# Kernel optimization log

Hardware: AMD Instinct MI355X
Metric: run time of the kernel (lower is better)

Reference implementation:

```python
import jax, jax.numpy as jnp
import numpy as np

N_NODES = 50000
N_EDGES = 800000
IN_DIM = 64
HID = 64
OUT_DIM = 40
NEG_SLOPE = 0.2


def _gat_layer(x, src, dst, W, b, att, bias, n_nodes):
    # x: [N, Fin] -> lin -> [N, Fout]; heads = 1
    h = x @ W.T + b
    x_i = h[dst]                      # [E, F] target features
    x_j = h[src]                      # [E, F] source features
    # edge attention logits: cat([x_i, x_j]) @ att.T -> [E, 1]
    alpha = jnp.concatenate([x_i, x_j], axis=-1) @ att.T
    alpha = jax.nn.leaky_relu(alpha, NEG_SLOPE)
    # segment softmax over destination node (pyg_utils.softmax)
    amax = jax.ops.segment_max(alpha, dst, num_segments=n_nodes)
    e = jnp.exp(alpha - amax[dst])
    denom = jax.ops.segment_sum(e, dst, num_segments=n_nodes)
    alpha = e / (denom[dst] + 1e-16)
    # message = alpha * x_j, aggr='add' scatter to dst, then + bias
    out = jax.ops.segment_sum(x_j * alpha, dst, num_segments=n_nodes)
    return out + bias


def setup_inputs() -> dict:
    key = jax.random.key(0)
    ks = jax.random.split(key, 12)
    x = jax.random.normal(ks[0], (N_NODES, IN_DIM), dtype=jnp.float32)
    edge_index = jax.random.randint(ks[1], (2, N_EDGES), 0, N_NODES, dtype=jnp.int64)
    def glorot(k, shape):
        fan_in, fan_out = shape[1], shape[0]
        lim = float(np.sqrt(6.0 / (fan_in + fan_out)))
        return jax.random.uniform(k, shape, jnp.float32, -lim, lim)
    W1 = glorot(ks[2], (HID, IN_DIM))
    b1 = jnp.zeros((HID,), jnp.float32)
    att1 = glorot(ks[3], (1, 2 * HID))
    bias1 = jnp.zeros((HID,), jnp.float32)
    W2 = glorot(ks[4], (HID, HID))
    b2 = jnp.zeros((HID,), jnp.float32)
    att2 = glorot(ks[5], (1, 2 * HID))
    bias2 = jnp.zeros((HID,), jnp.float32)
    Wp1 = glorot(ks[6], (HID, HID))
    bp1 = jnp.zeros((HID,), jnp.float32)
    Wp2 = glorot(ks[7], (OUT_DIM, HID))
    bp2 = jnp.zeros((OUT_DIM,), jnp.float32)
    return {"x": x, "edge_index": edge_index,
            "W1": W1, "b1": b1, "att1": att1, "bias1": bias1,
            "W2": W2, "b2": b2, "att2": att2, "bias2": bias2,
            "Wp1": Wp1, "bp1": bp1, "Wp2": Wp2, "bp2": bp2}


def reference(x, edge_index, W1, b1, att1, bias1, W2, b2, att2, bias2,
              Wp1, bp1, Wp2, bp2):
    src, dst = edge_index[0], edge_index[1]
    n = x.shape[0]
    # layer 1 (GAT) + relu; dropout p=0 in eval -> identity
    h = jax.nn.relu(_gat_layer(x, src, dst, W1, b1, att1, bias1, n))
    # layer 2 (GAT) + relu
    h = jax.nn.relu(_gat_layer(h, src, dst, W2, b2, att2, bias2, n))
    # post-MP MLP + log_softmax over classes
    h = h @ Wp1.T + bp1
    logits = h @ Wp2.T + bp2
    return jax.nn.log_softmax(logits, axis=1)
```

## Files before the change

### kernel.cpp

```cpp
#include <hip/hip_runtime.h>
#include <hip/hip_fp16.h>
#include <math.h>

#define NN 50000
#define NE 800000
#define NEG 0.2f

#define NPB 128
#define CHK 6250
#define NBUK 98
#define LCAP 10240
#define GB 782

typedef __attribute__((ext_vector_type(8))) short short8v;
typedef __attribute__((ext_vector_type(4))) float f32x4;

__device__ __forceinline__ float lrelu(float x){ return x > 0.f ? x : NEG * x; }

__device__ __forceinline__ float bcastf(float v, int l){
    return __uint_as_float(__builtin_amdgcn_readlane(__float_as_uint(v), l));
}
__device__ __forceinline__ short bf16t(float x){ return (short)(__float_as_uint(x) >> 16); }
__device__ __forceinline__ float bf16tof(short s){
    return __uint_as_float(((unsigned)(unsigned short)s) << 16);
}

__device__ __forceinline__ void lin_body(int blk, int tid,
                                         const float* __restrict__ X,
                                         const float* __restrict__ W,
                                         const float* __restrict__ b,
                                         const float* __restrict__ att,
                                         __half* __restrict__ Hh,
                                         float* __restrict__ ad,
                                         float* __restrict__ as_, int n){
    int lane = tid & 63, wid = tid >> 6;
    int nb = blk * 64 + wid * 16;
    if (nb >= n) return;
    int r0 = lane & 15, rg = lane >> 4;

    short8v a_hi[2], a_lo[2];
    int arow = nb + r0; if (arow >= n) arow = n - 1;
    const float* xp = X + (size_t)arow * 64 + rg * 8;
    #pragma unroll
    for (int ks = 0; ks < 2; ++ks){
        #pragma unroll
        for (int j = 0; j < 8; ++j){
            float v = xp[ks * 32 + j];
            short h = bf16t(v);
            a_hi[ks][j] = h;
            a_lo[ks][j] = bf16t(v - bf16tof(h));
        }
    }

    f32x4 acc[4] = {{0,0,0,0},{0,0,0,0},{0,0,0,0},{0,0,0,0}};
    #pragma unroll
    for (int nt = 0; nt < 4; ++nt){
        const float* wp = W + (size_t)(nt * 16 + r0) * 64 + rg * 8;
        #pragma unroll
        for (int ks = 0; ks < 2; ++ks){
            short8v b_hi, b_lo;
            #pragma unroll
            for (int j = 0; j < 8; ++j){
                float v = wp[ks * 32 + j];
                short h = bf16t(v);
                b_hi[j] = h;
                b_lo[j] = bf16t(v - bf16tof(h));
            }
            acc[nt] = __builtin_amdgcn_mfma_f32_16x16x32_bf16(a_hi[ks], b_hi, acc[nt], 0, 0, 0);
            acc[nt] = __builtin_amdgcn_mfma_f32_16x16x32_bf16(a_hi[ks], b_lo, acc[nt], 0, 0, 0);
            acc[nt] = __builtin_amdgcn_mfma_f32_16x16x32_bf16(a_lo[ks], b_hi, acc[nt], 0, 0, 0);
        }
    }

    #pragma unroll
    for (int nt = 0; nt < 4; ++nt){
        float bb = b[nt * 16 + r0];
        #pragma unroll
        for (int q = 0; q < 4; ++q){
            int node = nb + rg * 4 + q;
            float v = acc[nt][q] + bb;
            acc[nt][q] = v;
            if (node < n) Hh[(size_t)node * 64 + nt * 16 + r0] = __float2half(v);
        }
    }

    float attd[4], atts[4];
    #pragma unroll
    for (int nt = 0; nt < 4; ++nt){
        attd[nt] = att[nt * 16 + r0];
        atts[nt] = att[64 + nt * 16 + r0];
    }
    #pragma unroll
    for (int q = 0; q < 4; ++q){
        float pd = 0.f, ps = 0.f;
        #pragma unroll
        for (int nt = 0; nt < 4; ++nt){
            pd = fmaf(attd[nt], acc[nt][q], pd);
            ps = fmaf(atts[nt], acc[nt][q], ps);
        }
        #pragma unroll
        for (int off = 8; off; off >>= 1){
            pd += __shfl_xor(pd, off);
            ps += __shfl_xor(ps, off);
        }
        int node = nb + rg * 4 + q;
        if (r0 == 0 && node < n){ ad[node] = pd; as_[node] = ps; }
    }
}

__global__ __launch_bounds__(256) void k_fuse0(const float* __restrict__ X,
                                               const float* __restrict__ W1,
                                               const float* __restrict__ b1,
                                               const float* __restrict__ att1,
                                               __half* __restrict__ Hh,
                                               float* __restrict__ ad,
                                               float* __restrict__ as_,
                                               const int* __restrict__ dst,
                                               int* __restrict__ counts,
                                               const float* __restrict__ Wp1,
                                               const float* __restrict__ bp1,
                                               const float* __restrict__ Wp2,
                                               const float* __restrict__ bp2,
                                               float* __restrict__ Wc,
                                               float* __restrict__ bc){
    __shared__ int c[NBUK];
    int tid = threadIdx.x, blk = blockIdx.x;
    if (blk < GB){
        lin_body(blk, tid, X, W1, b1, att1, Hh, ad, as_, NN);
    } else if (blk < GB + NPB){
        int cb = blk - GB;
        for (int i = tid; i < NBUK; i += 256) c[i] = 0;
        __syncthreads();
        int beg = cb * CHK, end = min(beg + CHK, NE);
        for (int i = beg + tid; i < end; i += 256) atomicAdd(&c[dst[i] >> 9], 1);
        __syncthreads();
        for (int i = tid; i < NBUK; i += 256) counts[i * NPB + cb] = c[i];
    } else {
        for (int idx = tid; idx < 2560; idx += 256){
            int cc = idx >> 6, k = idx & 63;
            float s = 0.f;
            #pragma unroll 8
            for (int j = 0; j < 64; ++j) s = fmaf(Wp2[cc * 64 + j], Wp1[j * 64 + k], s);
            Wc[idx] = s;
        }
        if (tid < 40){
            float s = bp2[tid];
            for (int j = 0; j < 64; ++j) s = fmaf(Wp2[tid * 64 + j], bp1[j], s);
            bc[tid] = s;
        }
    }
}

__global__ __launch_bounds__(NPB) void k_scan1(int* __restrict__ counts,
                                               int* __restrict__ tot){
    __shared__ int wsum[2];
    int b = blockIdx.x, tid = threadIdx.x, lane = tid & 63, wid = tid >> 6;
    int v = counts[b * NPB + tid];
    int incl = v;
    #pragma unroll
    for (int off = 1; off < 64; off <<= 1){
        int t = __shfl_up(incl, off);
        if (lane >= off) incl += t;
    }
    if (lane == 63) wsum[wid] = incl;
    __syncthreads();
    int excl = incl - v + (wid ? wsum[0] : 0);
    counts[b * NPB + tid] = excl;
    if (tid == NPB - 1) tot[b] = excl + v;
}

__global__ __launch_bounds__(128) void k_scan2(const int* __restrict__ tot,
                                               int* __restrict__ bbase){
    __shared__ int wsum[2];
    int tid = threadIdx.x, lane = tid & 63, wid = tid >> 6;
    int v = (tid < NBUK) ? tot[tid] : 0;
    int incl = v;
    #pragma unroll
    for (int off = 1; off < 64; off <<= 1){
        int t = __shfl_up(incl, off);
        if (lane >= off) incl += t;
    }
    if (lane == 63) wsum[wid] = incl;
    __syncthreads();
    int excl = incl - v + (wid ? wsum[0] : 0);
    if (tid < NBUK) bbase[tid] = excl;
    if (tid == NBUK - 1) bbase[NBUK] = excl + v;
}

__global__ __launch_bounds__(256) void k_partC(const int* __restrict__ src,
                                               const int* __restrict__ dst,
                                               const int* __restrict__ cofs,
                                               const int* __restrict__ bbase,
                                               unsigned* __restrict__ part){
    __shared__ int lcur[NBUK];
    int tid = threadIdx.x, blk = blockIdx.x;
    for (int i = tid; i < NBUK; i += 256) lcur[i] = bbase[i] + cofs[i * NPB + blk];
    __syncthreads();
    int beg = blk * CHK, end = min(beg + CHK, NE);
    for (int i = beg + tid; i < end; i += 256){
        int d = dst[i];
        int pos = atomicAdd(&lcur[d >> 9], 1);
        part[pos] = ((unsigned)(d & 511) << 16) | (unsigned)src[i];
    }
}

__global__ __launch_bounds__(256) void k_buildD(const unsigned* __restrict__ part,
                                                const int* __restrict__ bbase,
                                                int* __restrict__ rowstart,
                                                int* __restrict__ csr){
    __shared__ int hist[512], cur[512];
    __shared__ int csrbuf[LCAP];
    __shared__ int swave[4];
    int tid = threadIdx.x, lane = tid & 63, wid = tid >> 6;
    int b = blockIdx.x;
    int ebeg = bbase[b], eend = bbase[b + 1], cnt = eend - ebeg;

    for (int i = tid; i < 512; i += 256) hist[i] = 0;
    __syncthreads();
    for (int i = tid; i < cnt; i += 256) atomicAdd(&hist[part[ebeg + i] >> 16], 1);
    __syncthreads();

    int h0 = hist[2 * tid], h1 = hist[2 * tid + 1];
    int v = h0 + h1, incl = v;
    #pragma unroll
    for (int off = 1; off < 64; off <<= 1){
        int t = __shfl_up(incl, off);
        if (lane >= off) incl += t;
    }
    if (lane == 63) swave[wid] = incl;
    __syncthreads();
    int woff = 0;
    #pragma unroll
    for (int w = 0; w < 4; ++w) if (w < wid) woff += swave[w];
    int e0 = woff + incl - v;
    int e1 = e0 + h0;
    cur[2 * tid] = e0; cur[2 * tid + 1] = e1;
    int gi = b * 512 + 2 * tid;
    if (gi     <= NN) rowstart[gi]     = ebeg + e0;
    if (gi + 1 <= NN) rowstart[gi + 1] = ebeg + e1;
    __syncthreads();

    for (int i = tid; i < cnt; i += 256){
        unsigned u = part[ebeg + i];
        int lp = atomicAdd(&cur[u >> 16], 1);
        if (lp < LCAP) csrbuf[lp] = (int)(u & 0xFFFFu);
    }
    __syncthreads();
    int m = min(cnt, LCAP);
    for (int i = tid; i < m; i += 256) csr[ebeg + i] = csrbuf[i];
}

__global__ __launch_bounds__(256) void k_lin_mfma(const float* __restrict__ X,
                                                  const float* __restrict__ W,
                                                  const float* __restrict__ b,
                                                  const float* __restrict__ att,
                                                  __half* __restrict__ Hh,
                                                  float* __restrict__ ad,
                                                  float* __restrict__ as_, int n){
    lin_body(blockIdx.x, threadIdx.x, X, W, b, att, Hh, ad, as_, n);
}

__global__ __launch_bounds__(256) void k_agg(const __half2* __restrict__ H2,
                                             const float* __restrict__ ad,
                                             const float* __restrict__ as_,
                                             const int* __restrict__ rowstart,
                                             const int* __restrict__ csr,
                                             const float2* __restrict__ bias2,
                                             float2* __restrict__ OUT2, int n){
    int tid = threadIdx.x, lane = tid & 63, wid = tid >> 6;
    int node = blockIdx.x * 4 + wid;
    if (node >= n) return;
    int beg = rowstart[node], end = rowstart[node + 1];
    float adn = ad[node];
    int half = lane >> 5, hl = lane & 31;

    float accx = 0.f, accy = 0.f, denom = 0.f;
    for (int cbeg = beg; cbeg < end; cbeg += 64){
        int k = cbeg + lane;
        int s = (k < end) ? csr[k] : 0;
        float e = (k < end) ? __expf(lrelu(adn + as_[s])) : 0.f;
        float es = e;
        #pragma unroll
        for (int off = 32; off; off >>= 1) es += __shfl_xor(es, off);
        denom += es;
        int cnt = min(64, end - cbeg);
        int j = 0;
        for (; j + 8 <= cnt; j += 8){
            int i0 = j + half, i1 = j + 2 + half, i2 = j + 4 + half, i3 = j + 6 + half;
            int   s0 = __shfl(s, i0), s1 = __shfl(s, i1), s2 = __shfl(s, i2), s3 = __shfl(s, i3);
            float e0 = __shfl(e, i0), e1 = __shfl(e, i1), e2 = __shfl(e, i2), e3 = __shfl(e, i3);
            __half2 ha = H2[(size_t)s0 * 32 + hl];
            __half2 hb = H2[(size_t)s1 * 32 + hl];
            __half2 hc = H2[(size_t)s2 * 32 + hl];
            __half2 hd = H2[(size_t)s3 * 32 + hl];
            float2 fa = __half22float2(ha), fb = __half22float2(hb);
            float2 fc = __half22float2(hc), fd = __half22float2(hd);
            accx = fmaf(e0, fa.x, accx); accy = fmaf(e0, fa.y, accy);
            accx = fmaf(e1, fb.x, accx); accy = fmaf(e1, fb.y, accy);
            accx = fmaf(e2, fc.x, accx); accy = fmaf(e2, fc.y, accy);
            accx = fmaf(e3, fd.x, accx); accy = fmaf(e3, fd.y, accy);
        }
        for (; j + 4 <= cnt; j += 4){
            int i0 = j + half, i1 = j + 2 + half;
            int   s0 = __shfl(s, i0), s1 = __shfl(s, i1);
            float e0 = __shfl(e, i0), e1 = __shfl(e, i1);
            float2 fa = __half22float2(H2[(size_t)s0 * 32 + hl]);
            float2 fb = __half22float2(H2[(size_t)s1 * 32 + hl]);
            accx = fmaf(e0, fa.x, accx); accy = fmaf(e0, fa.y, accy);
            accx = fmaf(e1, fb.x, accx); accy = fmaf(e1, fb.y, accy);
        }
        for (; j < cnt; j += 2){
            int idx = j + half;
            int   se = __shfl(s, idx);
            float ee = __shfl(e, idx);
            float2 f = __half22float2(H2[(size_t)se * 32 + hl]);
            accx = fmaf(ee, f.x, accx); accy = fmaf(ee, f.y, accy);
        }
    }
    accx += __shfl_xor(accx, 32);
    accy += __shfl_xor(accy, 32);
    if (half == 0){
        float2 bb = bias2[hl];
        float inv = 1.f / (denom + 1e-16f);
        float2 o;
        o.x = fmaxf(fmaf(accx, inv, bb.x), 0.f);
        o.y = fmaxf(fmaf(accy, inv, bb.y), 0.f);
        OUT2[(size_t)node * 32 + hl] = o;
    }
}

__global__ __launch_bounds__(256) void k_mlp_mfma(const float* __restrict__ G,
                                                  const float* __restrict__ Wc,
                                                  const float* __restrict__ bc,
                                                  float* __restrict__ out, int n){
    int lane = threadIdx.x & 63, wid = threadIdx.x >> 6;
    int nb = blockIdx.x * 64 + wid * 16;
    if (nb >= n) return;
    int r0 = lane & 15, rg = lane >> 4;

    short8v a_hi[2], a_lo[2];
    int arow = nb + r0; if (arow >= n) arow = n - 1;
    const float* gp = G + (size_t)arow * 64 + rg * 8;
    #pragma unroll
    for (int ks = 0; ks < 2; ++ks){
        #pragma unroll
        for (int j = 0; j < 8; ++j){
            float v = gp[ks * 32 + j];
            short h = bf16t(v);
            a_hi[ks][j] = h;
            a_lo[ks][j] = bf16t(v - bf16tof(h));
        }
    }

    f32x4 acc[3] = {{0,0,0,0},{0,0,0,0},{0,0,0,0}};
    #pragma unroll
    for (int nt = 0; nt < 3; ++nt){
        int f = nt * 16 + r0;
        int fr = (f < 40) ? f : 39;
        const float* wp = Wc + (size_t)fr * 64 + rg * 8;
        #pragma unroll
        for (int ks = 0; ks < 2; ++ks){
            short8v b_hi, b_lo;
            #pragma unroll
            for (int j = 0; j < 8; ++j){
                float v = wp[ks * 32 + j];
                short h = bf16t(v);
                b_hi[j] = h;
                b_lo[j] = bf16t(v - bf16tof(h));
            }
            acc[nt] = __builtin_amdgcn_mfma_f32_16x16x32_bf16(a_hi[ks], b_hi, acc[nt], 0, 0, 0);
            acc[nt] = __builtin_amdgcn_mfma_f32_16x16x32_bf16(a_hi[ks], b_lo, acc[nt], 0, 0, 0);
            acc[nt] = __builtin_amdgcn_mfma_f32_16x16x32_bf16(a_lo[ks], b_hi, acc[nt], 0, 0, 0);
        }
    }

    float bcv[3];
    #pragma unroll
    for (int nt = 0; nt < 3; ++nt){
        int f = nt * 16 + r0;
        bcv[nt] = (f < 40) ? bc[f] : 0.f;
    }

    #pragma unroll
    for (int q = 0; q < 4; ++q){
        int node = nb + rg * 4 + q;
        float l0 = acc[0][q] + bcv[0];
        float l1 = acc[1][q] + bcv[1];
        float l2 = (32 + r0 < 40) ? acc[2][q] + bcv[2] : -INFINITY;
        float m = fmaxf(l0, fmaxf(l1, l2));
        #pragma unroll
        for (int off = 8; off; off >>= 1) m = fmaxf(m, __shfl_xor(m, off));
        float s = __expf(l0 - m) + __expf(l1 - m) + ((32 + r0 < 40) ? __expf(l2 - m) : 0.f);
        #pragma unroll
        for (int off = 8; off; off >>= 1) s += __shfl_xor(s, off);
        float lse = m + __logf(s);
        if (node < n){
            out[(size_t)node * 40 + r0]      = l0 - lse;
            out[(size_t)node * 40 + 16 + r0] = l1 - lse;
            if (32 + r0 < 40) out[(size_t)node * 40 + 32 + r0] = l2 - lse;
        }
    }
}

extern "C" void kernel_launch(void* const* d_in, const int* in_sizes, int n_in,
                              void* d_out, int out_size, void* d_ws, size_t ws_size,
                              hipStream_t stream){
    const float* x     = (const float*)d_in[0];
    const int*   ei    = (const int*)  d_in[1];
    const float* W1    = (const float*)d_in[2];
    const float* b1    = (const float*)d_in[3];
    const float* att1  = (const float*)d_in[4];
    const float* bias1 = (const float*)d_in[5];
    const float* W2    = (const float*)d_in[6];
    const float* b2    = (const float*)d_in[7];
    const float* att2  = (const float*)d_in[8];
    const float* bias2 = (const float*)d_in[9];
    const float* Wp1   = (const float*)d_in[10];
    const float* bp1   = (const float*)d_in[11];
    const float* Wp2   = (const float*)d_in[12];
    const float* bp2   = (const float*)d_in[13];
    float* out = (float*)d_out;

    float*    base     = (float*)d_ws;
    float*    g        = base;
    __half*   hh       = (__half*)(base + 3200000);
    unsigned* part     = (unsigned*)(base + 4800000);
    int*      csr      = (int*)(base + 5600000);
    int*      counts   = (int*)(base + 6400000);
    int*      tot      = (int*)(base + 6412944);
    int*      bbase    = (int*)(base + 6413072);
    int*      rowstart = (int*)(base + 6413200);
    float*    ad       = base + 6463208;
    float*    as_      = base + 6513208;
    float*    Wc       = base + 6563208;
    float*    bc       = base + 6565768;

    const int* srcv = ei;
    const int* dstv = ei + NE;

    k_fuse0 <<<GB + NPB + 1, 256, 0, stream>>>(x, W1, b1, att1, hh, ad, as_,
                                               dstv, counts,
                                               Wp1, bp1, Wp2, bp2, Wc, bc);
    k_scan1 <<<NBUK, NPB, 0, stream>>>(counts, tot);
    k_scan2 <<<1, 128, 0, stream>>>(tot, bbase);
    k_partC <<<NPB, 256, 0, stream>>>(srcv, dstv, counts, bbase, part);
    k_buildD<<<NBUK, 256, 0, stream>>>(part, bbase, rowstart, csr);

    int nb = (NN + 3) / 4;
    k_agg     <<<nb, 256, 0, stream>>>((const __half2*)hh, ad, as_, rowstart, csr,
                                       (const float2*)bias1, (float2*)g, NN);
    k_lin_mfma<<<GB, 256, 0, stream>>>(g, W2, b2, att2, hh, ad, as_, NN);
    k_agg     <<<nb, 256, 0, stream>>>((const __half2*)hh, ad, as_, rowstart, csr,
                                       (const float2*)bias2, (float2*)g, NN);
    k_mlp_mfma<<<GB, 256, 0, stream>>>(g, Wc, bc, out, NN);
}
```

Before: 146.7 us.

## Fold bucket-base scan into partition kernels and stage edge data in LDS

Removes the single-block k_scan2 launch by having k_partC and k_buildD each recompute the 98-entry bucket base prefix sum redundantly in shared memory. In the aggregation kernel, per-edge source indices and attention weights are written to LDS and read back instead of broadcast with shuffles. The inner tail loops are collapsed into one 8-step loop that relies on zero-padded entries. This saves a kernel launch and some shuffle instructions, at the cost of redundant scan work per block and extra LDS traffic. Padded slots gather row 0 with weight zero, adding some wasted loads.

New measurement: 142.1 us. 3.1% less time.

```diff
diff --git a/kernel.cpp b/kernel.cpp
--- a/kernel.cpp
+++ b/kernel.cpp
@@ -17,9 +17,6 @@
 
 __device__ __forceinline__ float lrelu(float x){ return x > 0.f ? x : NEG * x; }
 
-__device__ __forceinline__ float bcastf(float v, int l){
-    return __uint_as_float(__builtin_amdgcn_readlane(__float_as_uint(v), l));
-}
 __device__ __forceinline__ short bf16t(float x){ return (short)(__float_as_uint(x) >> 16); }
 __device__ __forceinline__ float bf16tof(short s){
     return __uint_as_float(((unsigned)(unsigned short)s) << 16);
@@ -169,32 +166,36 @@
     if (tid == NPB - 1) tot[b] = excl + v;
 }
 
-__global__ __launch_bounds__(128) void k_scan2(const int* __restrict__ tot,
-                                               int* __restrict__ bbase){
-    __shared__ int wsum[2];
-    int tid = threadIdx.x, lane = tid & 63, wid = tid >> 6;
-    int v = (tid < NBUK) ? tot[tid] : 0;
-    int incl = v;
-    #pragma unroll
-    for (int off = 1; off < 64; off <<= 1){
-        int t = __shfl_up(incl, off);
-        if (lane >= off) incl += t;
-    }
-    if (lane == 63) wsum[wid] = incl;
-    __syncthreads();
-    int excl = incl - v + (wid ? wsum[0] : 0);
-    if (tid < NBUK) bbase[tid] = excl;
-    if (tid == NBUK - 1) bbase[NBUK] = excl + v;
+__device__ __forceinline__ void bbase_scan(const int* __restrict__ tot,
+                                           int* bb, int* wsum, int tid){
+    int lane = tid & 63, w2 = tid >> 6;
+    int vv = 0, incl = 0;
+    if (tid < 128){
+        vv = (tid < NBUK) ? tot[tid] : 0;
+        incl = vv;
+        #pragma unroll
+        for (int off = 1; off < 64; off <<= 1){
+            int t = __shfl_up(incl, off);
+            if (lane >= off) incl += t;
+        }
+        if (lane == 63) wsum[w2] = incl;
+    }
+    __syncthreads();
+    if (tid < NBUK) bb[tid] = incl - vv + (w2 ? wsum[0] : 0);
+    __syncthreads();
 }
 
 __global__ __launch_bounds__(256) void k_partC(const int* __restrict__ src,
                                                const int* __restrict__ dst,
                                                const int* __restrict__ cofs,
-                                               const int* __restrict__ bbase,
+                                               const int* __restrict__ tot,
                                                unsigned* __restrict__ part){
     __shared__ int lcur[NBUK];
+    __shared__ int bb[NBUK];
+    __shared__ int wsum[2];
     int tid = threadIdx.x, blk = blockIdx.x;
-    for (int i = tid; i < NBUK; i += 256) lcur[i] = bbase[i] + cofs[i * NPB + blk];
+    bbase_scan(tot, bb, wsum, tid);
+    for (int i = tid; i < NBUK; i += 256) lcur[i] = bb[i] + cofs[i * NPB + blk];
     __syncthreads();
     int beg = blk * CHK, end = min(beg + CHK, NE);
     for (int i = beg + tid; i < end; i += 256){
@@ -205,15 +206,18 @@
 }
 
 __global__ __launch_bounds__(256) void k_buildD(const unsigned* __restrict__ part,
-                                                const int* __restrict__ bbase,
+                                                const int* __restrict__ tot,
                                                 int* __restrict__ rowstart,
                                                 int* __restrict__ csr){
     __shared__ int hist[512], cur[512];
     __shared__ int csrbuf[LCAP];
     __shared__ int swave[4];
+    __shared__ int bb[NBUK];
+    __shared__ int wsum2[2];
     int tid = threadIdx.x, lane = tid & 63, wid = tid >> 6;
     int b = blockIdx.x;
-    int ebeg = bbase[b], eend = bbase[b + 1], cnt = eend - ebeg;
+    bbase_scan(tot, bb, wsum2, tid);
+    int ebeg = bb[b], cnt = tot[b];
 
     for (int i = tid; i < 512; i += 256) hist[i] = 0;
     __syncthreads();
@@ -267,6 +271,8 @@
                                              const int* __restrict__ csr,
                                              const float2* __restrict__ bias2,
                                              float2* __restrict__ OUT2, int n){
+    __shared__ float e_sh[4][64];
+    __shared__ int   s_sh[4][64];
     int tid = threadIdx.x, lane = tid & 63, wid = tid >> 6;
     int node = blockIdx.x * 4 + wid;
     if (node >= n) return;
@@ -277,44 +283,30 @@
     float accx = 0.f, accy = 0.f, denom = 0.f;
     for (int cbeg = beg; cbeg < end; cbeg += 64){
         int k = cbeg + lane;
-        int s = (k < end) ? csr[k] : 0;
-        float e = (k < end) ? __expf(lrelu(adn + as_[s])) : 0.f;
+        bool valid = (k < end);
+        int s = valid ? csr[k] : 0;
+        float e = valid ? __expf(lrelu(adn + as_[s])) : 0.f;
+        e_sh[wid][lane] = e;
+        s_sh[wid][lane] = valid ? s : 0;
         float es = e;
         #pragma unroll
         for (int off = 32; off; off >>= 1) es += __shfl_xor(es, off);
         denom += es;
         int cnt = min(64, end - cbeg);
-        int j = 0;
-        for (; j + 8 <= cnt; j += 8){
+        for (int j = 0; j < cnt; j += 8){
             int i0 = j + half, i1 = j + 2 + half, i2 = j + 4 + half, i3 = j + 6 + half;
-            int   s0 = __shfl(s, i0), s1 = __shfl(s, i1), s2 = __shfl(s, i2), s3 = __shfl(s, i3);
-            float e0 = __shfl(e, i0), e1 = __shfl(e, i1), e2 = __shfl(e, i2), e3 = __shfl(e, i3);
-            __half2 ha = H2[(size_t)s0 * 32 + hl];
-            __half2 hb = H2[(size_t)s1 * 32 + hl];
-            __half2 hc = H2[(size_t)s2 * 32 + hl];
-            __half2 hd = H2[(size_t)s3 * 32 + hl];
-            float2 fa = __half22float2(ha), fb = __half22float2(hb);
-            float2 fc = __half22float2(hc), fd = __half22float2(hd);
+            int   s0 = s_sh[wid][i0], s1 = s_sh[wid][i1];
+            int   s2 = s_sh[wid][i2], s3 = s_sh[wid][i3];
+            float e0 = e_sh[wid][i0], e1 = e_sh[wid][i1];
+            float e2 = e_sh[wid][i2], e3 = e_sh[wid][i3];
+            float2 fa = __half22float2(H2[(size_t)s0 * 32 + hl]);
+            float2 fb = __half22float2(H2[(size_t)s1 * 32 + hl]);
+            float2 fc = __half22float2(H2[(size_t)s2 * 32 + hl]);
+            float2 fd = __half22float2(H2[(size_t)s3 * 32 + hl]);
             accx = fmaf(e0, fa.x, accx); accy = fmaf(e0, fa.y, accy);
             accx = fmaf(e1, fb.x, accx); accy = fmaf(e1, fb.y, accy);
             accx = fmaf(e2, fc.x, accx); accy = fmaf(e2, fc.y, accy);
             accx = fmaf(e3, fd.x, accx); accy = fmaf(e3, fd.y, accy);
-        }
-        for (; j + 4 <= cnt; j += 4){
-            int i0 = j + half, i1 = j + 2 + half;
-            int   s0 = __shfl(s, i0), s1 = __shfl(s, i1);
-            float e0 = __shfl(e, i0), e1 = __shfl(e, i1);
-            float2 fa = __half22float2(H2[(size_t)s0 * 32 + hl]);
-            float2 fb = __half22float2(H2[(size_t)s1 * 32 + hl]);
-            accx = fmaf(e0, fa.x, accx); accy = fmaf(e0, fa.y, accy);
-            accx = fmaf(e1, fb.x, accx); accy = fmaf(e1, fb.y, accy);
-        }
-        for (; j < cnt; j += 2){
-            int idx = j + half;
-            int   se = __shfl(s, idx);
-            float ee = __shfl(e, idx);
-            float2 f = __half22float2(H2[(size_t)se * 32 + hl]);
-            accx = fmaf(ee, f.x, accx); accy = fmaf(ee, f.y, accy);
         }
     }
     accx += __shfl_xor(accx, 32);
@@ -428,7 +420,6 @@
     int*      csr      = (int*)(base + 5600000);
     int*      counts   = (int*)(base + 6400000);
     int*      tot      = (int*)(base + 6412944);
-    int*      bbase    = (int*)(base + 6413072);
     int*      rowstart = (int*)(base + 6413200);
     float*    ad       = base + 6463208;
     float*    as_      = base + 6513208;
@@ -442,9 +433,8 @@
                                                dstv, counts,
                                                Wp1, bp1, Wp2, bp2, Wc, bc);
     k_scan1 <<<NBUK, NPB, 0, stream>>>(counts, tot);
-    k_scan2 <<<1, 128, 0, stream>>>(tot, bbase);
-    k_partC <<<NPB, 256, 0, stream>>>(srcv, dstv, counts, bbase, part);
-    k_buildD<<<NBUK, 256, 0, stream>>>(part, bbase, rowstart, csr);
+    k_partC <<<NPB, 256, 0, stream>>>(srcv, dstv, counts, tot, part);
+    k_buildD<<<NBUK, 256, 0, stream>>>(part, tot, rowstart, csr);
 
     int nb = (NN + 3) / 4;
     k_agg     <<<nb, 256, 0, stream>>>((const __half2*)hh, ad, as_, rowstart, csr,
```
